# Performance work log

Measured on AMD Instinct MI355X. Metric: run time of the kernel, lower is better.

The kernel has to match this reference:

```python
import jax, jax.numpy as jnp
import numpy as np

N_NODES = 100000
N_EDGES = 1600000
FEAT_DIM = 256
EMBED_DIM = 256


def setup_inputs() -> dict:
    key = jax.random.key(0)
    k1, k2, k3, k4, k5 = jax.random.split(key, 5)
    x = jax.random.normal(k1, (N_NODES, FEAT_DIM), dtype=jnp.float32)
    # Xavier-uniform init for weight [embed_dim, feat_dim]
    limit = float(np.sqrt(6.0 / (EMBED_DIM + FEAT_DIM)))
    weight = jax.random.uniform(k2, (EMBED_DIM, FEAT_DIM), dtype=jnp.float32,
                                minval=-limit, maxval=limit)
    edge_src = jax.random.randint(k3, (N_EDGES,), 0, N_NODES, dtype=jnp.int32)
    edge_dst = jnp.sort(jax.random.randint(k4, (N_EDGES,), 0, N_NODES, dtype=jnp.int32))
    # normalized adjacency values (e.g. D^-1/2 A D^-1/2 entries), positive
    edge_val = jax.random.uniform(k5, (N_EDGES,), dtype=jnp.float32)
    return {"x": x, "weight": weight, "edge_src": edge_src,
            "edge_dst": edge_dst, "edge_val": edge_val}


def reference(x, weight, edge_src, edge_dst, edge_val):
    # Fused GeMM + SpMM: out = A @ (x @ W^T)
    h = jnp.einsum('nf,ef->ne', x, weight)          # [N, embed_dim] dense GEMM
    msgs = h[edge_src] * edge_val[:, None]          # [E, embed_dim] gather + scale
    out = jax.ops.segment_sum(msgs, edge_dst, num_segments=x.shape[0])  # SpMM scatter-add
    return out
```

## Files before the change

### kernel.cpp

```cpp
#include <hip/hip_runtime.h>

#define FEAT 256
#define EMB 256

typedef __attribute__((ext_vector_type(4))) float f32x4;
typedef __attribute__((ext_vector_type(8))) short short8;

__device__ __forceinline__ unsigned cvtpk(float lo, float hi) {
    unsigned r;
    asm volatile("v_cvt_pk_bf16_f32 %0, %1, %2" : "=v"(r) : "v"(lo), "v"(hi));
    return r;
}

__global__ __launch_bounds__(512) void gemm_q8(
    const float* __restrict__ X, const float* __restrict__ W,
    unsigned* __restrict__ H32, float* __restrict__ S, int M) {
    __shared__ ushort As[128][32];
    __shared__ ushort Bs[256][32];

    const int t    = threadIdx.x;
    const int lane = t & 63;
    const int wave = t >> 6;
    const int wr   = (wave >> 2) * 64;
    const int wc   = (wave & 3) * 64;
    const int m0   = blockIdx.x * 128;

    f32x4 acc[4][4] = {};

    const int srow = t >> 3;
    const int sc4  = (t & 7) * 4;

    for (int k0 = 0; k0 < FEAT; k0 += 32) {
        __syncthreads();
        #pragma unroll
        for (int j = 0; j < 2; ++j) {
            int row = srow + 64 * j;
            int gr  = m0 + row;
            f32x4 v = {0.f, 0.f, 0.f, 0.f};
            if (gr < M) v = *(const f32x4*)(X + (size_t)gr * FEAT + k0 + sc4);
            uint2 u = {cvtpk(v.x, v.y), cvtpk(v.z, v.w)};
            *(uint2*)&As[row][sc4] = u;
        }
        #pragma unroll
        for (int j = 0; j < 4; ++j) {
            int row = srow + 64 * j;
            f32x4 wv = *(const f32x4*)(W + (size_t)row * FEAT + k0 + sc4);
            uint2 uw = {cvtpk(wv.x, wv.y), cvtpk(wv.z, wv.w)};
            *(uint2*)&Bs[row][sc4] = uw;
        }
        __syncthreads();

        const int r  = lane & 15;
        const int kr = (lane >> 4) * 8;
        short8 a[4], b[4];
        #pragma unroll
        for (int i = 0; i < 4; ++i) a[i] = *(const short8*)&As[wr + i * 16 + r][kr];
        #pragma unroll
        for (int j = 0; j < 4; ++j) b[j] = *(const short8*)&Bs[wc + j * 16 + r][kr];
        #pragma unroll
        for (int i = 0; i < 4; ++i)
            #pragma unroll
            for (int j = 0; j < 4; ++j)
                acc[i][j] = __builtin_amdgcn_mfma_f32_16x16x32_bf16(a[i], b[j], acc[i][j], 0, 0, 0);
    }

    const int g  = lane >> 4;
    const int cc = lane & 15;
    const int b  = wave & 3;
    #pragma unroll
    for (int i = 0; i < 4; ++i) {
        #pragma unroll
        for (int q = 0; q < 4; ++q) {
            const int row = m0 + wr + i * 16 + g * 4 + q;
            float mx = fmaxf(fmaxf(fabsf(acc[i][0][q]), fabsf(acc[i][1][q])),
                             fmaxf(fabsf(acc[i][2][q]), fabsf(acc[i][3][q])));
            mx = fmaxf(mx, __shfl_xor(mx, 1, 64));
            mx = fmaxf(mx, __shfl_xor(mx, 2, 64));
            mx = fmaxf(mx, __shfl_xor(mx, 4, 64));
            mx = fmaxf(mx, __shfl_xor(mx, 8, 64));
            const float inv = mx > 1e-30f ? 127.0f * __builtin_amdgcn_rcpf(mx) : 0.0f;
            if (row < M) {
                unsigned wdw = 0;
                #pragma unroll
                for (int j = 0; j < 4; ++j) {
                    int u = (int)fmaf(acc[i][j][q], inv, 128.5f);
                    u = u < 0 ? 0 : (u > 255 ? 255 : u);
                    wdw |= (unsigned)u << (8 * j);
                }
                H32[(size_t)row * 64 + b * 16 + cc] = wdw;
                if (cc == 0) S[(size_t)row * 4 + b] = mx * (1.0f / 127.0f);
            }
        }
    }
}

__global__ __launch_bounds__(256) void build_rowptr(
    const int* __restrict__ dst, int* __restrict__ rp, int E, int N) {
    int e = blockIdx.x * 256 + threadIdx.x;
    if (e >= E) return;
    int d    = dst[e];
    int prev = (e == 0) ? -1 : dst[e - 1];
    for (int n = prev + 1; n <= d; ++n) rp[n] = e;
    if (e == E - 1) {
        for (int n = d + 1; n <= N; ++n) rp[n] = E;
    }
}

__global__ __launch_bounds__(256) void spmm_q8(
    const uint4* __restrict__ H16, const float* __restrict__ S,
    const int* __restrict__ rp, const int* __restrict__ src,
    const float* __restrict__ val, float* __restrict__ out, int M) {
    const int lane = threadIdx.x & 63;
    const int wave = threadIdx.x >> 6;
    const int li   = lane & 15;
    const int grp  = lane >> 4;
    const int b    = li >> 2;
    const int node = blockIdx.x * 16 + wave * 4 + grp;
    if (node >= M) return;
    const int lo = rp[node], hi = rp[node + 1];

    float a0[16], a1[16];
    #pragma unroll
    for (int k = 0; k < 16; ++k) { a0[k] = 0.f; a1[k] = 0.f; }
    float corr0 = 0.f, corr1 = 0.f;

    for (int e = lo; e < hi; e += 2) {
        const int e1 = e + 1;
        const int c1 = e1 < hi ? e1 : e;
        const int s0 = src[e], s1 = src[c1];
        const float v0 = val[e];
        float v1 = e1 < hi ? val[c1] : 0.f;
        const float vs0 = v0 * S[(size_t)s0 * 4 + b];
        const float vs1 = v1 * S[(size_t)s1 * 4 + b];
        const uint4 p0 = H16[(size_t)s0 * 16 + li];
        const uint4 p1 = H16[(size_t)s1 * 16 + li];
        corr0 += vs0;
        corr1 += vs1;
        const unsigned pd0[4] = {p0.x, p0.y, p0.z, p0.w};
        const unsigned pd1[4] = {p1.x, p1.y, p1.z, p1.w};
        #pragma unroll
        for (int d = 0; d < 4; ++d) {
            #pragma unroll
            for (int j = 0; j < 4; ++j) {
                a0[d * 4 + j] += vs0 * (float)((pd0[d] >> (8 * j)) & 0xffu);
                a1[d * 4 + j] += vs1 * (float)((pd1[d] >> (8 * j)) & 0xffu);
            }
        }
    }

    const float corr = (corr0 + corr1) * 128.0f;
    float* const obase = out + (size_t)node * EMB + b * 64 + (li & 3) * 4;
    #pragma unroll
    for (int j = 0; j < 4; ++j) {
        f32x4 o = {a0[j]      + a1[j]      - corr,
                   a0[4 + j]  + a1[4 + j]  - corr,
                   a0[8 + j]  + a1[8 + j]  - corr,
                   a0[12 + j] + a1[12 + j] - corr};
        __builtin_nontemporal_store(o, (f32x4*)(obase + j * 16));
    }
}

extern "C" void kernel_launch(void* const* d_in, const int* in_sizes, int n_in,
                              void* d_out, int out_size, void* d_ws, size_t ws_size,
                              hipStream_t stream) {
    const float* x    = (const float*)d_in[0];
    const float* w    = (const float*)d_in[1];
    const int*   esrc = (const int*)d_in[2];
    const int*   edst = (const int*)d_in[3];
    const float* eval = (const float*)d_in[4];

    const int M = in_sizes[0] / FEAT;
    const int E = in_sizes[2];

    unsigned* Hbuf = (unsigned*)d_ws;
    float*    S    = (float*)((char*)d_ws + (size_t)M * 256);
    int*      rp   = (int*)((char*)S + (size_t)M * 4 * sizeof(float));

    gemm_q8<<<(M + 127) / 128, 512, 0, stream>>>(x, w, Hbuf, S, M);
    build_rowptr<<<(E + 255) / 256, 256, 0, stream>>>(edst, rp, E, M);
    spmm_q8<<<(M + 15) / 16, 256, 0, stream>>>((const uint4*)Hbuf, S, rp, esrc, eval,
                                               (float*)d_out, M);
}
```

Measured before the change: 144.6 us.

## Pre-convert weights to bf16 with async LDS loads; unroll SpMM edge loop by four

A small prep kernel converts W to bf16 once, and the GEMM then loads the B tile straight into LDS with global_load_lds 16-byte async loads. This removes the per-block fp32 W loads and conversions. The SpMM loop now handles four edges per iteration so more gathers are in flight. The cost is an extra kernel launch and higher register pressure in the SpMM.

```diff
diff --git a/kernel.cpp b/kernel.cpp
--- a/kernel.cpp
+++ b/kernel.cpp
@@ -12,8 +12,22 @@
     return r;
 }
 
+__device__ __forceinline__ void async_b16(const void* g, void* l) {
+    __builtin_amdgcn_global_load_lds(
+        (const __attribute__((address_space(1))) unsigned*)g,
+        (__attribute__((address_space(3))) unsigned*)l, 16, 0, 0);
+}
+
+__global__ __launch_bounds__(256) void wprep(const float* __restrict__ W,
+                                             ushort* __restrict__ Wb) {
+    const int i = (blockIdx.x * 256 + threadIdx.x) * 4;
+    f32x4 v = *(const f32x4*)(W + i);
+    uint2 u = {cvtpk(v.x, v.y), cvtpk(v.z, v.w)};
+    *(uint2*)(Wb + i) = u;
+}
+
 __global__ __launch_bounds__(512) void gemm_q8(
-    const float* __restrict__ X, const float* __restrict__ W,
+    const float* __restrict__ X, const ushort* __restrict__ Wb,
     unsigned* __restrict__ H32, float* __restrict__ S, int M) {
     __shared__ ushort As[128][32];
     __shared__ ushort Bs[256][32];
@@ -30,8 +44,16 @@
     const int srow = t >> 3;
     const int sc4  = (t & 7) * 4;
 
+    const int brow0 = wave * 16 + (lane >> 2);
+    const int bcol  = (lane & 3) * 8;
+
     for (int k0 = 0; k0 < FEAT; k0 += 32) {
         __syncthreads();
+        #pragma unroll
+        for (int c = 0; c < 2; ++c) {
+            const ushort* src = Wb + (size_t)(c * 128 + brow0) * FEAT + k0 + bcol;
+            async_b16(src, &Bs[c * 128 + wave * 16][0]);
+        }
         #pragma unroll
         for (int j = 0; j < 2; ++j) {
             int row = srow + 64 * j;
@@ -40,13 +62,6 @@
             if (gr < M) v = *(const f32x4*)(X + (size_t)gr * FEAT + k0 + sc4);
             uint2 u = {cvtpk(v.x, v.y), cvtpk(v.z, v.w)};
             *(uint2*)&As[row][sc4] = u;
-        }
-        #pragma unroll
-        for (int j = 0; j < 4; ++j) {
-            int row = srow + 64 * j;
-            f32x4 wv = *(const f32x4*)(W + (size_t)row * FEAT + k0 + sc4);
-            uint2 uw = {cvtpk(wv.x, wv.y), cvtpk(wv.z, wv.w)};
-            *(uint2*)&Bs[row][sc4] = uw;
         }
         __syncthreads();
 
@@ -122,40 +137,50 @@
     float a0[16], a1[16];
     #pragma unroll
     for (int k = 0; k < 16; ++k) { a0[k] = 0.f; a1[k] = 0.f; }
-    float corr0 = 0.f, corr1 = 0.f;
-
-    for (int e = lo; e < hi; e += 2) {
-        const int e1 = e + 1;
-        const int c1 = e1 < hi ? e1 : e;
-        const int s0 = src[e], s1 = src[c1];
+    float corr = 0.f;
+
+    for (int e = lo; e < hi; e += 4) {
+        const int c1 = e + 1 < hi ? e + 1 : e;
+        const int c2 = e + 2 < hi ? e + 2 : e;
+        const int c3 = e + 3 < hi ? e + 3 : e;
+        const int s0 = src[e], s1 = src[c1], s2 = src[c2], s3 = src[c3];
         const float v0 = val[e];
-        float v1 = e1 < hi ? val[c1] : 0.f;
+        const float v1 = e + 1 < hi ? val[c1] : 0.f;
+        const float v2 = e + 2 < hi ? val[c2] : 0.f;
+        const float v3 = e + 3 < hi ? val[c3] : 0.f;
         const float vs0 = v0 * S[(size_t)s0 * 4 + b];
         const float vs1 = v1 * S[(size_t)s1 * 4 + b];
+        const float vs2 = v2 * S[(size_t)s2 * 4 + b];
+        const float vs3 = v3 * S[(size_t)s3 * 4 + b];
         const uint4 p0 = H16[(size_t)s0 * 16 + li];
         const uint4 p1 = H16[(size_t)s1 * 16 + li];
-        corr0 += vs0;
-        corr1 += vs1;
-        const unsigned pd0[4] = {p0.x, p0.y, p0.z, p0.w};
-        const unsigned pd1[4] = {p1.x, p1.y, p1.z, p1.w};
+        const uint4 p2 = H16[(size_t)s2 * 16 + li];
+        const uint4 p3 = H16[(size_t)s3 * 16 + li];
+        corr += (vs0 + vs1) + (vs2 + vs3);
+        const unsigned q0[4] = {p0.x, p0.y, p0.z, p0.w};
+        const unsigned q1[4] = {p1.x, p1.y, p1.z, p1.w};
+        const unsigned q2[4] = {p2.x, p2.y, p2.z, p2.w};
+        const unsigned q3[4] = {p3.x, p3.y, p3.z, p3.w};
         #pragma unroll
         for (int d = 0; d < 4; ++d) {
             #pragma unroll
             for (int j = 0; j < 4; ++j) {
-                a0[d * 4 + j] += vs0 * (float)((pd0[d] >> (8 * j)) & 0xffu);
-                a1[d * 4 + j] += vs1 * (float)((pd1[d] >> (8 * j)) & 0xffu);
+                a0[d * 4 + j] += vs0 * (float)((q0[d] >> (8 * j)) & 0xffu)
+                               + vs2 * (float)((q2[d] >> (8 * j)) & 0xffu);
+                a1[d * 4 + j] += vs1 * (float)((q1[d] >> (8 * j)) & 0xffu)
+                               + vs3 * (float)((q3[d] >> (8 * j)) & 0xffu);
             }
         }
     }
 
-    const float corr = (corr0 + corr1) * 128.0f;
+    const float corrs = corr * 128.0f;
     float* const obase = out + (size_t)node * EMB + b * 64 + (li & 3) * 4;
     #pragma unroll
     for (int j = 0; j < 4; ++j) {
-        f32x4 o = {a0[j]      + a1[j]      - corr,
-                   a0[4 + j]  + a1[4 + j]  - corr,
-                   a0[8 + j]  + a1[8 + j]  - corr,
-                   a0[12 + j] + a1[12 + j] - corr};
+        f32x4 o = {a0[j]      + a1[j]      - corrs,
+                   a0[4 + j]  + a1[4 + j]  - corrs,
+                   a0[8 + j]  + a1[8 + j]  - corrs,
+                   a0[12 + j] + a1[12 + j] - corrs};
         __builtin_nontemporal_store(o, (f32x4*)(obase + j * 16));
     }
 }
@@ -175,8 +200,12 @@
     unsigned* Hbuf = (unsigned*)d_ws;
     float*    S    = (float*)((char*)d_ws + (size_t)M * 256);
     int*      rp   = (int*)((char*)S + (size_t)M * 4 * sizeof(float));
-
-    gemm_q8<<<(M + 127) / 128, 512, 0, stream>>>(x, w, Hbuf, S, M);
+    size_t    woff = (size_t)M * 256 + (size_t)M * 16 + (size_t)(M + 1) * 4;
+    woff = (woff + 255) & ~(size_t)255;
+    ushort*   Wb   = (ushort*)((char*)d_ws + woff);
+
+    wprep<<<(EMB * FEAT / 4 + 255) / 256, 256, 0, stream>>>(w, Wb);
+    gemm_q8<<<(M + 127) / 128, 512, 0, stream>>>(x, Wb, Hbuf, S, M);
     build_rowptr<<<(E + 255) / 256, 256, 0, stream>>>(edst, rp, E, M);
     spmm_q8<<<(M + 15) / 16, 256, 0, stream>>>((const uint4*)Hbuf, S, rp, esrc, eval,
                                                (float*)d_out, M);
```

After: 157.8 us. 1.09x slower.

## Enlarge GEMM tile to 256 rows and prefetch next K slice into registers

Applied to the files above, without the earlier changes.

The GEMM block grows to 1024 threads covering 256 rows, so each W tile staged in shared memory is reused across twice as many X rows. Each thread now loads 8 contiguous floats per k-step, and the loads for the next k-slice are issued into registers before the MFMA loop so global latency overlaps compute. The cost is more registers per thread at 1024-thread blocks, possible occupancy limits, and half as many blocks (about 391) across the CUs.

```diff
diff --git a/kernel.cpp b/kernel.cpp
--- a/kernel.cpp
+++ b/kernel.cpp
@@ -12,10 +12,10 @@
     return r;
 }
 
-__global__ __launch_bounds__(512) void gemm_q8(
+__global__ __launch_bounds__(1024) void gemm_q8(
     const float* __restrict__ X, const float* __restrict__ W,
     unsigned* __restrict__ H32, float* __restrict__ S, int M) {
-    __shared__ ushort As[128][32];
+    __shared__ ushort As[256][32];
     __shared__ ushort Bs[256][32];
 
     const int t    = threadIdx.x;
@@ -23,35 +23,47 @@
     const int wave = t >> 6;
     const int wr   = (wave >> 2) * 64;
     const int wc   = (wave & 3) * 64;
-    const int m0   = blockIdx.x * 128;
+    const int m0   = blockIdx.x * 256;
 
     f32x4 acc[4][4] = {};
 
-    const int srow = t >> 3;
-    const int sc4  = (t & 7) * 4;
+    const int srow = t >> 2;
+    const int sc8  = (t & 3) * 8;
+    const int gr   = m0 + srow;
+    const bool inr = gr < M;
+    const float* const xp = X + (size_t)gr * FEAT + sc8;
+    const float* const wp = W + (size_t)srow * FEAT + sc8;
+
+    const int r  = lane & 15;
+    const int kr = (lane >> 4) * 8;
+
+    f32x4 xv0 = {0.f, 0.f, 0.f, 0.f}, xv1 = {0.f, 0.f, 0.f, 0.f};
+    f32x4 wv0, wv1;
+    if (inr) { xv0 = *(const f32x4*)xp; xv1 = *(const f32x4*)(xp + 4); }
+    wv0 = *(const f32x4*)wp;
+    wv1 = *(const f32x4*)(wp + 4);
 
     for (int k0 = 0; k0 < FEAT; k0 += 32) {
         __syncthreads();
-        #pragma unroll
-        for (int j = 0; j < 2; ++j) {
-            int row = srow + 64 * j;
-            int gr  = m0 + row;
-            f32x4 v = {0.f, 0.f, 0.f, 0.f};
-            if (gr < M) v = *(const f32x4*)(X + (size_t)gr * FEAT + k0 + sc4);
-            uint2 u = {cvtpk(v.x, v.y), cvtpk(v.z, v.w)};
-            *(uint2*)&As[row][sc4] = u;
-        }
-        #pragma unroll
-        for (int j = 0; j < 4; ++j) {
-            int row = srow + 64 * j;
-            f32x4 wv = *(const f32x4*)(W + (size_t)row * FEAT + k0 + sc4);
-            uint2 uw = {cvtpk(wv.x, wv.y), cvtpk(wv.z, wv.w)};
-            *(uint2*)&Bs[row][sc4] = uw;
+        {
+            uint4 ux = {cvtpk(xv0.x, xv0.y), cvtpk(xv0.z, xv0.w),
+                        cvtpk(xv1.x, xv1.y), cvtpk(xv1.z, xv1.w)};
+            uint4 uw = {cvtpk(wv0.x, wv0.y), cvtpk(wv0.z, wv0.w),
+                        cvtpk(wv1.x, wv1.y), cvtpk(wv1.z, wv1.w)};
+            *(uint4*)&As[srow][sc8] = ux;
+            *(uint4*)&Bs[srow][sc8] = uw;
         }
         __syncthreads();
 
-        const int r  = lane & 15;
-        const int kr = (lane >> 4) * 8;
+        if (k0 + 32 < FEAT) {
+            const int kn = k0 + 32;
+            xv0 = {0.f, 0.f, 0.f, 0.f};
+            xv1 = {0.f, 0.f, 0.f, 0.f};
+            if (inr) { xv0 = *(const f32x4*)(xp + kn); xv1 = *(const f32x4*)(xp + kn + 4); }
+            wv0 = *(const f32x4*)(wp + kn);
+            wv1 = *(const f32x4*)(wp + kn + 4);
+        }
+
         short8 a[4], b[4];
         #pragma unroll
         for (int i = 0; i < 4; ++i) a[i] = *(const short8*)&As[wr + i * 16 + r][kr];
@@ -176,7 +188,7 @@
     float*    S    = (float*)((char*)d_ws + (size_t)M * 256);
     int*      rp   = (int*)((char*)S + (size_t)M * 4 * sizeof(float));
 
-    gemm_q8<<<(M + 127) / 128, 512, 0, stream>>>(x, w, Hbuf, S, M);
+    gemm_q8<<<(M + 255) / 256, 1024, 0, stream>>>(x, w, Hbuf, S, M);
     build_rowptr<<<(E + 255) / 256, 256, 0, stream>>>(edst, rp, E, M);
     spmm_q8<<<(M + 15) / 16, 256, 0, stream>>>((const uint4*)Hbuf, S, rp, esrc, eval,
                                                (float*)d_out, M);
```

Result: faster. 140.2 us (-3.0%).
